# Kernel optimization log

Hardware: AMD Instinct MI355X
Metric: run time of the kernel (lower is better)

## Reference

```python
import jax, jax.numpy as jnp
import numpy as np

V, D, H, L, B, S = 32000, 512, 512, 2, 64, 64
PAD = 0
NEG = -1000000000.0


def setup_inputs() -> dict:
    key = jax.random.key(0)
    ks = jax.random.split(key, 12)
    s = 0.05
    X = jax.random.randint(ks[0], (B, S), 0, V)
    enc = jax.random.normal(ks[1], (B, S - 1, H), jnp.float32)
    mask = jnp.zeros((S - 1, S - 1), dtype=bool)
    emb = jax.random.normal(ks[2], (V, D), jnp.float32) * s
    lstm_Wih = jax.random.normal(ks[3], (L, 4 * H, D), jnp.float32) * s  # D == H so stacking works for layer>0
    lstm_Whh = jax.random.normal(ks[4], (L, 4 * H, H), jnp.float32) * s
    lstm_bih = jax.random.normal(ks[5], (L, 4 * H), jnp.float32) * s
    lstm_bhh = jax.random.normal(ks[6], (L, 4 * H), jnp.float32) * s
    attn_Wh = jax.random.normal(ks[7], (H, H), jnp.float32) * s  # attn weight cols acting on decoder hidden
    attn_We = jax.random.normal(ks[8], (H, H), jnp.float32) * s  # attn weight cols acting on encoder outputs
    attn_b = jax.random.normal(ks[9], (H,), jnp.float32) * s
    v_w = jax.random.normal(ks[10], (H,), jnp.float32) * s
    fc_W = jax.random.normal(ks[11], (V, 2 * H), jnp.float32) * s
    fc_b = jnp.zeros((V,), jnp.float32)
    return {"X": X, "encoderOutputs": enc, "mask": mask, "emb": emb,
            "lstm_Wih": lstm_Wih, "lstm_Whh": lstm_Whh, "lstm_bih": lstm_bih, "lstm_bhh": lstm_bhh,
            "attn_Wh": attn_Wh, "attn_We": attn_We, "attn_b": attn_b, "v_w": v_w,
            "fc_W": fc_W, "fc_b": fc_b}


def _forward(X, enc, mask, emb, Wih, Whh, bih, bhh, attn_Wh, attn_We, attn_b, v_w, fc_W, fc_b):
    Bn, Sn = X.shape
    T = Sn - 1
    E = emb[X[:, :-1]]  # [B,T,D]
    # encoder part of attention projection is time-invariant: hoist out of the loop
    enc_proj = jnp.einsum('beh,kh->bek', enc, attn_We) + attn_b  # [B,T,H]
    h0 = jnp.zeros((L, Bn, H), E.dtype)
    c0 = jnp.zeros((L, Bn, H), E.dtype)
    xs = (jnp.transpose(E, (1, 0, 2)), X[:, 1:].T, jnp.arange(T))

    def step(carry, x_t):
        h, c = carry
        e_t, tgt, t = x_t
        inp = e_t
        hs, cs = [], []
        for l in range(L):  # fixed small layer loop
            g = inp @ Wih[l].T + h[l] @ Whh[l].T + bih[l] + bhh[l]
            i, f, gg, o = jnp.split(g, 4, axis=-1)  # torch gate order i,f,g,o
            cn = jax.nn.sigmoid(f) * c[l] + jax.nn.sigmoid(i) * jnp.tanh(gg)
            hn = jax.nn.sigmoid(o) * jnp.tanh(cn)
            hs.append(hn); cs.append(cn)
            inp = hn
        h = jnp.stack(hs); c = jnp.stack(cs)
        top = inp  # [B,H] == LSTM output of last layer
        energy = jnp.tanh((top @ attn_Wh.T)[:, None, :] + enc_proj)  # [B,T,H]
        scores = energy @ v_w  # [B,T]
        # original: self.mask[t-1] (python negative wrap) then mask.unsqueeze(0).unsqueeze(1)
        m = mask[(t - 1) % mask.shape[0], :T]  # [T]
        s3 = jnp.where(m[None, None, :], NEG, scores[None])  # broadcast -> [1,B,T]
        att = jax.nn.softmax(s3, axis=1)[0]  # softmax over batch dim, as in original
        weighted = jnp.einsum('be,beh->bh', att, enc)
        logits = jnp.concatenate([top, weighted], axis=1) @ fc_W.T + fc_b  # [B,V]
        logp = jax.nn.log_softmax(logits, axis=-1)
        nll = -jnp.take_along_axis(logp, tgt[:, None], axis=1)[:, 0]
        valid = tgt != PAD
        loss_t = jnp.sum(jnp.where(valid, nll, 0.0)) / jnp.sum(valid)  # CE mean with ignore_index
        return (h, c), loss_t

    _, losses = jax.lax.scan(step, (h0, c0), xs)
    return jnp.mean(losses)  # totalLoss / (seq_len - 1)


def reference(X, encoderOutputs, mask, emb, lstm_Wih, lstm_Whh, lstm_bih, lstm_bhh, attn_Wh, attn_We, attn_b, v_w, fc_W, fc_b):
    return _forward(X, encoderOutputs, mask, emb, lstm_Wih, lstm_Whh, lstm_bih, lstm_bhh, attn_Wh, attn_We, attn_b, v_w, fc_W, fc_b)
```

## Files before the change

kernel.cpp:

```cpp
#include <hip/hip_runtime.h>
#include <math.h>

#define NEGV -1000000000.0f

typedef unsigned short u16;
typedef __attribute__((ext_vector_type(8))) short bf16x8;
typedef __attribute__((ext_vector_type(4))) float f32x4;

__device__ __forceinline__ u16 f2bf(float f){
  union { float f; unsigned u; } v; v.f = f;
  unsigned u = v.u;
  unsigned r = (u + 0x7fffu + ((u >> 16) & 1u)) >> 16;
  return (u16)r;
}
__device__ __forceinline__ float bf2f(u16 b){
  union { unsigned u; float f; } v; v.u = ((unsigned)b) << 16;
  return v.f;
}
__device__ __forceinline__ float sigmf(float x){ return 1.f / (1.f + __expf(-x)); }
__device__ __forceinline__ float tanhf_(float x){
  float e = __expf(-2.f * fabsf(x));
  float t = (1.f - e) / (1.f + e);
  return x >= 0.f ? t : -t;
}
__device__ __forceinline__ float wred64(float v){
  #pragma unroll
  for (int m = 32; m; m >>= 1) v += __shfl_xor(v, m, 64);
  return v;
}
__device__ __forceinline__ float wmax64(float v){
  #pragma unroll
  for (int m = 32; m; m >>= 1) v = fmaxf(v, __shfl_xor(v, m, 64));
  return v;
}

typedef const __attribute__((address_space(1))) unsigned int* gas_ptr;
typedef __attribute__((address_space(3))) unsigned int* las_ptr;
__device__ __forceinline__ void gl_lds16(const u16* g, u16* l){
  __builtin_amdgcn_global_load_lds((gas_ptr)g, (las_ptr)l, 16, 0, 0);
}

__device__ __forceinline__ void st_sc1_u16(u16* p, unsigned v){
  asm volatile("global_store_short %0, %1, off sc1" :: "v"(p), "v"(v) : "memory");
}

__global__ __launch_bounds__(256) void k_prep(
    const float* wih, const float* whh, const float* we, const float* wh,
    const float* fcw, const float* enc, const float* bih, const float* bhh,
    u16* wihb, u16* whhb, u16* web, u16* whb, u16* fcwb, u16* encb, float* b01)
{
  const long n0 = 2097152, n1 = 2097152, n2 = 262144, n3 = 262144;
  const long n4 = 32768000, n5 = 2064384, n6 = 4096;
  const long total = n0 + n1 + n2 + n3 + n4 + n5 + n6;
  long stride = (long)gridDim.x * 256;
  for (long i = (long)blockIdx.x * 256 + threadIdx.x; i < total; i += stride){
    long j = i;
    if (j < n0){ wihb[j] = f2bf(wih[j]); continue; } j -= n0;
    if (j < n1){ whhb[j] = f2bf(whh[j]); continue; } j -= n1;
    if (j < n2){ web[j]  = f2bf(we[j]);  continue; } j -= n2;
    if (j < n3){ whb[j]  = f2bf(wh[j]);  continue; } j -= n3;
    if (j < n4){ fcwb[j] = f2bf(fcw[j]); continue; } j -= n4;
    if (j < n5){ encb[j] = f2bf(enc[j]); continue; } j -= n5;
    b01[j] = bih[j] + bhh[j];
  }
}

__global__ __launch_bounds__(256) void k_embed(const int* X, const float* emb, u16* ebf){
  int row = blockIdx.x;
  int t = row >> 6, b = row & 63;
  int tok = X[b * 64 + t];
  const float* src = emb + (long)tok * 512;
  u16* dst = ebf + (long)row * 512;
  for (int j = threadIdx.x; j < 512; j += 256) dst[j] = f2bf(src[j]);
}

__global__ __launch_bounds__(256) void gemm_bt(
    const u16* Am, int lda, const u16* Bm, int ldb,
    float* C, int ldc, const float* bias, int K)
{
  __shared__ u16 sA[64 * 32], sB[64 * 32];
  int tm = blockIdx.x, tn = blockIdx.y;
  int tid = threadIdx.x;
  int wave = tid >> 6, lane = tid & 63;
  int wm = wave >> 1, wn = wave & 1;
  int q = lane >> 4, cl = lane & 15;
  f32x4 acc[2][2];
  #pragma unroll
  for (int i = 0; i < 2; i++)
    #pragma unroll
    for (int j = 0; j < 2; j++) acc[i][j] = (f32x4){0.f, 0.f, 0.f, 0.f};

  int r = tid >> 2, ck = tid & 3;
  const u16* Ags = Am + (long)(tm * 64 + r) * lda + ck * 8;
  const u16* Bgs = Bm + (long)(tn * 64 + r) * ldb + ck * 8;
  u16* sAw = &sA[wave * 512];
  u16* sBw = &sB[wave * 512];

  for (int kt = 0; kt < K; kt += 32){
    gl_lds16(Ags + kt, sAw);
    gl_lds16(Bgs + kt, sBw);
    __syncthreads();
    #pragma unroll
    for (int i = 0; i < 2; i++){
      bf16x8 af = *(const bf16x8*)&sA[(wm * 32 + i * 16 + cl) * 32 + q * 8];
      #pragma unroll
      for (int j = 0; j < 2; j++){
        bf16x8 bfv = *(const bf16x8*)&sB[(wn * 32 + j * 16 + cl) * 32 + q * 8];
        acc[i][j] = __builtin_amdgcn_mfma_f32_16x16x32_bf16(af, bfv, acc[i][j], 0, 0, 0);
      }
    }
    __syncthreads();
  }
  #pragma unroll
  for (int i = 0; i < 2; i++)
    #pragma unroll
    for (int j = 0; j < 2; j++){
      int colg = tn * 64 + wn * 32 + j * 16 + cl;
      float bv = bias ? bias[colg] : 0.f;
      #pragma unroll
      for (int rr = 0; rr < 4; rr++){
        int rowg = tm * 64 + wm * 32 + i * 16 + q * 4 + rr;
        C[(long)rowg * ldc + colg] = acc[i][j][rr] + bv;
      }
    }
}

__global__ __launch_bounds__(256) void gemm_btb(
    const u16* Am, int lda, const u16* Bm, int ldb,
    u16* C, int ldc, const float* bias, int K)
{
  __shared__ u16 sA[64 * 32], sB[64 * 32];
  int tm = blockIdx.x, tn = blockIdx.y;
  int tid = threadIdx.x;
  int wave = tid >> 6, lane = tid & 63;
  int wm = wave >> 1, wn = wave & 1;
  int q = lane >> 4, cl = lane & 15;
  f32x4 acc[2][2];
  #pragma unroll
  for (int i = 0; i < 2; i++)
    #pragma unroll
    for (int j = 0; j < 2; j++) acc[i][j] = (f32x4){0.f, 0.f, 0.f, 0.f};

  int r = tid >> 2, ck = tid & 3;
  const u16* Ags = Am + (long)(tm * 64 + r) * lda + ck * 8;
  const u16* Bgs = Bm + (long)(tn * 64 + r) * ldb + ck * 8;
  u16* sAw = &sA[wave * 512];
  u16* sBw = &sB[wave * 512];

  for (int kt = 0; kt < K; kt += 32){
    gl_lds16(Ags + kt, sAw);
    gl_lds16(Bgs + kt, sBw);
    __syncthreads();
    #pragma unroll
    for (int i = 0; i < 2; i++){
      bf16x8 af = *(const bf16x8*)&sA[(wm * 32 + i * 16 + cl) * 32 + q * 8];
      #pragma unroll
      for (int j = 0; j < 2; j++){
        bf16x8 bfv = *(const bf16x8*)&sB[(wn * 32 + j * 16 + cl) * 32 + q * 8];
        acc[i][j] = __builtin_amdgcn_mfma_f32_16x16x32_bf16(af, bfv, acc[i][j], 0, 0, 0);
      }
    }
    __syncthreads();
  }
  #pragma unroll
  for (int i = 0; i < 2; i++)
    #pragma unroll
    for (int j = 0; j < 2; j++){
      int colg = tn * 64 + wn * 32 + j * 16 + cl;
      float bv = bias ? bias[colg] : 0.f;
      #pragma unroll
      for (int rr = 0; rr < 4; rr++){
        int rowg = tm * 64 + wm * 32 + i * 16 + q * 4 + rr;
        C[(long)rowg * ldc + colg] = f2bf(acc[i][j][rr] + bv);
      }
    }
}

__device__ __forceinline__ void wait_flags(int* flags, int tid, int need0, int need1){
  if (tid < 64){
    int need = (tid < 32) ? need0 : need1;
    for (;;){
      int v = __hip_atomic_load(flags + tid, __ATOMIC_RELAXED, __HIP_MEMORY_SCOPE_AGENT);
      if (__ballot(v >= need) == ~0ull) break;
    }
  }
  __syncthreads();
}

#define LOAD_RING_FRAGS(afr, Ab)                                              \
  {                                                                            \
    _Pragma("unroll")                                                          \
    for (int kt = 0; kt < 16; kt++)                                            \
      asm volatile("global_load_dwordx4 %0, %1, off offset:%2 sc1"             \
                   : "=v"(afr[kt]) : "v"(Ab), "i"(kt * 64));                   \
    asm volatile("s_waitcnt vmcnt(0)" ::: "memory");                           \
    __builtin_amdgcn_sched_barrier(0);                                         \
  }

__global__ __launch_bounds__(256, 1) void lstm_pipe(
    const u16* whh0, const u16* wih1, const u16* whh1,
    const u16* x0b, const float* b1s,
    u16* ring0, u16* ring1, u16* feat, int* flags)
{
  __shared__ u16 sW[32768];
  __shared__ u16 sW2[32768];
  int wg = blockIdx.x;
  int layer = wg >> 5;
  int cc = (wg & 31) * 16;
  int tid = threadIdx.x;
  int wave = tid >> 6, lane = tid & 63;
  int q = lane >> 4, cl = lane & 15;
  int j = cc + cl;

  {
    const u16* src = layer ? whh1 : whh0;
    for (int ch = tid; ch < 4096; ch += 256){
      int row = ch >> 6, c = ch & 63;
      int g = row >> 4, r = row & 15;
      *(uint4*)&sW[((c * 4 + g) * 16 + r) * 8] =
          *(const uint4*)&src[(long)(g * 512 + cc + r) * 512 + c * 8];
      if (layer)
        *(uint4*)&sW2[((c * 4 + g) * 16 + r) * 8] =
            *(const uint4*)&wih1[(long)(g * 512 + cc + r) * 512 + c * 8];
    }
  }
  __syncthreads();

  float cst[4] = {0.f, 0.f, 0.f, 0.f};
  float bg[4];
  if (layer){
    #pragma unroll
    for (int g = 0; g < 4; g++) bg[g] = b1s[g * 512 + j];
  }

  const int LOW = -(1 << 30);

  for (int t = 0; t < 63; t++){
    f32x4 acc[4];
    #pragma unroll
    for (int g = 0; g < 4; g++) acc[g] = (f32x4){0.f, 0.f, 0.f, 0.f};

    if (layer == 0){
      float xg[4][4];
      #pragma unroll
      for (int rr = 0; rr < 4; rr++){
        int s = wave * 16 + q * 4 + rr;
        const u16* xr = x0b + (long)(t * 64 + s) * 2048 + j;
        #pragma unroll
        for (int g = 0; g < 4; g++) xg[g][rr] = bf2f(xr[g * 512]);
      }
      wait_flags(flags, tid, t, t - 3);
      {
        const u16* Ab = ring0 + ((t + 3) & 3) * 32768 + (wave * 16 + cl) * 512 + q * 8;
        bf16x8 afr[16];
        LOAD_RING_FRAGS(afr, Ab);
        #pragma unroll
        for (int kt = 0; kt < 16; kt++)
          #pragma unroll
          for (int g = 0; g < 4; g++){
            bf16x8 bfv = *(const bf16x8*)&sW[(((kt * 4 + q) * 4 + g) * 16 + cl) * 8];
            acc[g] = __builtin_amdgcn_mfma_f32_16x16x32_bf16(afr[kt], bfv, acc[g], 0, 0, 0);
          }
      }
      u16* hn = ring0 + (t & 3) * 32768;
      #pragma unroll
      for (int rr = 0; rr < 4; rr++){
        int s = wave * 16 + q * 4 + rr;
        float gi = acc[0][rr] + xg[0][rr];
        float gf = acc[1][rr] + xg[1][rr];
        float gg = acc[2][rr] + xg[2][rr];
        float go = acc[3][rr] + xg[3][rr];
        float cn = sigmf(gf) * cst[rr] + sigmf(gi) * tanhf_(gg);
        cst[rr] = cn;
        st_sc1_u16(hn + s * 512 + j, (unsigned)f2bf(sigmf(go) * tanhf_(cn)));
      }
    } else {
      wait_flags(flags, tid, LOW, t);
      {
        const u16* Ab = ring1 + ((t + 3) & 3) * 32768 + (wave * 16 + cl) * 512 + q * 8;
        bf16x8 afr[16];
        LOAD_RING_FRAGS(afr, Ab);
        #pragma unroll
        for (int kt = 0; kt < 16; kt++)
          #pragma unroll
          for (int g = 0; g < 4; g++){
            bf16x8 bfv = *(const bf16x8*)&sW[(((kt * 4 + q) * 4 + g) * 16 + cl) * 8];
            acc[g] = __builtin_amdgcn_mfma_f32_16x16x32_bf16(afr[kt], bfv, acc[g], 0, 0, 0);
          }
      }
      wait_flags(flags, tid, t + 1, LOW);
      {
        const u16* Ab = ring0 + (t & 3) * 32768 + (wave * 16 + cl) * 512 + q * 8;
        bf16x8 afr[16];
        LOAD_RING_FRAGS(afr, Ab);
        #pragma unroll
        for (int kt = 0; kt < 16; kt++)
          #pragma unroll
          for (int g = 0; g < 4; g++){
            bf16x8 bfv = *(const bf16x8*)&sW2[(((kt * 4 + q) * 4 + g) * 16 + cl) * 8];
            acc[g] = __builtin_amdgcn_mfma_f32_16x16x32_bf16(afr[kt], bfv, acc[g], 0, 0, 0);
          }
      }
      u16* hn = ring1 + (t & 3) * 32768;
      #pragma unroll
      for (int rr = 0; rr < 4; rr++){
        int s = wave * 16 + q * 4 + rr;
        float gi = acc[0][rr] + bg[0];
        float gf = acc[1][rr] + bg[1];
        float gg = acc[2][rr] + bg[2];
        float go = acc[3][rr] + bg[3];
        float cn = sigmf(gf) * cst[rr] + sigmf(gi) * tanhf_(gg);
        cst[rr] = cn;
        u16 hb = f2bf(sigmf(go) * tanhf_(cn));
        st_sc1_u16(hn + s * 512 + j, (unsigned)hb);
        feat[(long)(t * 64 + s) * 1024 + j] = hb;
      }
    }
    asm volatile("s_waitcnt vmcnt(0)" ::: "memory");
    __syncthreads();
    if (tid == 0)
      __hip_atomic_store(flags + wg, t + 1, __ATOMIC_RELAXED, __HIP_MEMORY_SCOPE_AGENT);
  }
}

__global__ __launch_bounds__(256) void k_scores(
    const float* qb, const float* encp, const float* vw, float* scores)
{
  int row = blockIdx.x;
  int b = row & 63;
  int wave = threadIdx.x >> 6, lane = threadIdx.x & 63;
  float qv[8], vwv[8];
  const float* qr = qb + (long)row * 512 + lane * 8;
  #pragma unroll
  for (int i = 0; i < 8; i++){ qv[i] = qr[i]; vwv[i] = vw[lane * 8 + i]; }
  for (int e = wave; e < 63; e += 4){
    const float* er = encp + (long)(b * 63 + e) * 512 + lane * 8;
    float s = 0.f;
    #pragma unroll
    for (int i = 0; i < 8; i++) s += vwv[i] * tanhf_(qv[i] + er[i]);
    s = wred64(s);
    if (lane == 0) scores[(long)row * 63 + e] = s;
  }
}

__global__ __launch_bounds__(64) void k_att(float* scores, const unsigned char* mask){
  int idx = blockIdx.x;
  int t = idx / 63, e = idx - t * 63;
  int lane = threadIdx.x;
  long off = (long)(t * 64 + lane) * 63 + e;
  float s = scores[off];
  if (mask[((t + 62) % 63) * 63 + e]) s = NEGV;
  float M = wmax64(s);
  float p = __expf(s - M);
  float S = wred64(p);
  scores[off] = p / S;
}

__global__ __launch_bounds__(256) void k_weighted(
    const float* att, const float* enc, u16* feat)
{
  int row = blockIdx.x;
  int b = row & 63;
  int j = threadIdx.x;
  float a0 = 0.f, a1 = 0.f;
  const float* ar = att + (long)row * 63;
  const float* er = enc + (long)b * 63 * 512;
  for (int e = 0; e < 63; e++){
    float a = ar[e];
    a0 += a * er[(long)e * 512 + j];
    a1 += a * er[(long)e * 512 + j + 256];
  }
  feat[(long)row * 1024 + 512 + j] = f2bf(a0);
  feat[(long)row * 1024 + 768 + j] = f2bf(a1);
}

__global__ __launch_bounds__(256) void gemm_fc(
    const u16* Am, const u16* Bm, const float* fcb, float* partials)
{
  __shared__ u16 sA[128 * 32], sB[128 * 32];
  __shared__ float sm[128][2], ss[128][2];
  int tm = blockIdx.x, tn = blockIdx.y;
  int tid = threadIdx.x;
  int wave = tid >> 6, lane = tid & 63;
  int wm = wave >> 1, wn = wave & 1;
  int q = lane >> 4, cl = lane & 15;
  f32x4 acc[4][4];
  #pragma unroll
  for (int i = 0; i < 4; i++)
    #pragma unroll
    for (int j = 0; j < 4; j++) acc[i][j] = (f32x4){0.f, 0.f, 0.f, 0.f};

  const u16 *Ag[2], *Bg[2];
  u16 *sAd[2], *sBd[2];
  #pragma unroll
  for (int h = 0; h < 2; h++){
    int idx = h * 256 + tid, rr = idx >> 2, ck = idx & 3;
    Ag[h] = Am + (long)(tm * 128 + rr) * 1024 + ck * 8;
    Bg[h] = Bm + (long)(tn * 128 + rr) * 1024 + ck * 8;
    sAd[h] = &sA[(h * 4 + wave) * 512];
    sBd[h] = &sB[(h * 4 + wave) * 512];
  }
  for (int kt = 0; kt < 1024; kt += 32){
    #pragma unroll
    for (int h = 0; h < 2; h++){
      gl_lds16(Ag[h] + kt, sAd[h]);
      gl_lds16(Bg[h] + kt, sBd[h]);
    }
    __syncthreads();
    bf16x8 afr[4];
    #pragma unroll
    for (int mt = 0; mt < 4; mt++)
      afr[mt] = *(const bf16x8*)&sA[(wm * 64 + mt * 16 + cl) * 32 + q * 8];
    #pragma unroll
    for (int nt = 0; nt < 4; nt++){
      bf16x8 bfv = *(const bf16x8*)&sB[(wn * 64 + nt * 16 + cl) * 32 + q * 8];
      #pragma unroll
      for (int mt = 0; mt < 4; mt++)
        acc[mt][nt] = __builtin_amdgcn_mfma_f32_16x16x32_bf16(afr[mt], bfv, acc[mt][nt], 0, 0, 0);
    }
    __syncthreads();
  }
  float fb[4];
  #pragma unroll
  for (int nt = 0; nt < 4; nt++) fb[nt] = fcb[tn * 128 + wn * 64 + nt * 16 + cl];
  #pragma unroll
  for (int mt = 0; mt < 4; mt++){
    #pragma unroll
    for (int rr = 0; rr < 4; rr++){
      float vals[4];
      float vm = -3.0e38f, vs = 0.f;
      #pragma unroll
      for (int nt = 0; nt < 4; nt++){ float v = acc[mt][nt][rr] + fb[nt]; vals[nt] = v; vm = fmaxf(vm, v); }
      #pragma unroll
      for (int nt = 0; nt < 4; nt++) vs += __expf(vals[nt] - vm);
      #pragma unroll
      for (int m = 1; m < 16; m <<= 1){
        float om = __shfl_xor(vm, m, 16);
        float os = __shfl_xor(vs, m, 16);
        float nm = fmaxf(vm, om);
        vs = vs * __expf(vm - nm) + os * __expf(om - nm);
        vm = nm;
      }
      if (cl == 0){ int rl = wm * 64 + mt * 16 + q * 4 + rr; sm[rl][wn] = vm; ss[rl][wn] = vs; }
    }
  }
  __syncthreads();
  if (tid < 128){
    float m0 = sm[tid][0], m1 = sm[tid][1];
    float M = fmaxf(m0, m1);
    float S = ss[tid][0] * __expf(m0 - M) + ss[tid][1] * __expf(m1 - M);
    long row = tm * 128 + tid;
    partials[(row * 250 + tn) * 2]     = M;
    partials[(row * 250 + tn) * 2 + 1] = S;
  }
}

__global__ __launch_bounds__(256) void k_rowstats(
    const float* partials, const u16* feat, const u16* fcwb,
    const float* fcb, const int* X, float* nll)
{
  int row = blockIdx.x * 4 + (threadIdx.x >> 6);
  int lane = threadIdx.x & 63;
  if (row >= 4032) return;
  float vm = -3.0e38f, vs = 0.f;
  const float* pr = partials + (long)row * 500;
  for (int i = lane; i < 250; i += 64){
    float m = pr[i * 2], s2 = pr[i * 2 + 1];
    float nm = fmaxf(vm, m);
    vs = vs * __expf(vm - nm) + s2 * __expf(m - nm);
    vm = nm;
  }
  #pragma unroll
  for (int m = 32; m; m >>= 1){
    float om = __shfl_xor(vm, m, 64);
    float os = __shfl_xor(vs, m, 64);
    float nm = fmaxf(vm, om);
    vs = vs * __expf(vm - nm) + os * __expf(om - nm);
    vm = nm;
  }
  float logZ = vm + __logf(vs);
  int t = row >> 6, b = row & 63;
  int tgt = X[b * 64 + t + 1];
  const u16* fr = feat + (long)row * 1024 + lane * 16;
  const u16* wr = fcwb + (long)tgt * 1024 + lane * 16;
  float d = 0.f;
  #pragma unroll
  for (int i = 0; i < 16; i++) d += bf2f(fr[i]) * bf2f(wr[i]);
  d = wred64(d);
  if (lane == 0) nll[row] = logZ - (d + fcb[tgt]);
}

__global__ __launch_bounds__(256) void k_final(const float* nll, const int* X, float* out){
  __shared__ float lt[64];
  int wave = threadIdx.x >> 6, lane = threadIdx.x & 63;
  for (int t = wave; t < 63; t += 4){
    int tgt = X[lane * 64 + t + 1];
    float v = (tgt != 0) ? nll[t * 64 + lane] : 0.f;
    float c = (tgt != 0) ? 1.f : 0.f;
    v = wred64(v); c = wred64(c);
    if (lane == 0) lt[t] = v / c;
  }
  __syncthreads();
  if (threadIdx.x == 0){
    float s = 0.f;
    for (int t = 0; t < 63; t++) s += lt[t];
    out[0] = s / 63.f;
  }
}

extern "C" void kernel_launch(void* const* d_in, const int* in_sizes, int n_in,
                              void* d_out, int out_size, void* d_ws, size_t ws_size,
                              hipStream_t stream)
{
  (void)in_sizes; (void)n_in; (void)out_size; (void)ws_size;
  const int*   X    = (const int*)d_in[0];
  const float* enc  = (const float*)d_in[1];
  const unsigned char* mask = (const unsigned char*)d_in[2];
  const float* emb  = (const float*)d_in[3];
  const float* wih  = (const float*)d_in[4];
  const float* whh  = (const float*)d_in[5];
  const float* bih  = (const float*)d_in[6];
  const float* bhh  = (const float*)d_in[7];
  const float* awh  = (const float*)d_in[8];
  const float* awe  = (const float*)d_in[9];
  const float* ab   = (const float*)d_in[10];
  const float* vw   = (const float*)d_in[11];
  const float* fcw  = (const float*)d_in[12];
  const float* fcb  = (const float*)d_in[13];
  float* out = (float*)d_out;

  char* w = (char*)d_ws;
  size_t o = 0;
  auto alloc = [&](size_t bytes){ size_t r = o; o = (o + bytes + 255) & ~(size_t)255; return r; };
  size_t o_ebf  = alloc((size_t)4032 * 512 * 2);
  size_t o_wihb = alloc((size_t)2 * 2048 * 512 * 2);
  size_t o_whhb = alloc((size_t)2 * 2048 * 512 * 2);
  size_t o_web  = alloc((size_t)512 * 512 * 2);
  size_t o_whb  = alloc((size_t)512 * 512 * 2);
  size_t o_fcwb = alloc((size_t)32000 * 1024 * 2);
  size_t o_encb = alloc((size_t)4032 * 512 * 2);
  size_t o_b01  = alloc((size_t)4096 * 4);
  size_t o_x0   = alloc((size_t)4032 * 2048 * 2);
  size_t o_encp = alloc((size_t)4032 * 512 * 4);
  size_t o_q    = alloc((size_t)4032 * 512 * 4);
  size_t o_feat = alloc((size_t)4096 * 1024 * 2);
  size_t o_ring = alloc((size_t)2 * 4 * 32768 * 2);
  size_t o_flags= alloc((size_t)256);
  size_t o_sc   = alloc((size_t)63 * 64 * 63 * 4);
  size_t o_part = alloc((size_t)4096 * 250 * 2 * 4);
  size_t o_nll  = alloc((size_t)4032 * 4);

  u16* ebf   = (u16*)(w + o_ebf);
  u16* wihb  = (u16*)(w + o_wihb);
  u16* whhb  = (u16*)(w + o_whhb);
  u16* web   = (u16*)(w + o_web);
  u16* whb   = (u16*)(w + o_whb);
  u16* fcwb  = (u16*)(w + o_fcwb);
  u16* encb  = (u16*)(w + o_encb);
  float* b01 = (float*)(w + o_b01);
  u16* x0b   = (u16*)(w + o_x0);
  float* encp= (float*)(w + o_encp);
  float* qb  = (float*)(w + o_q);
  u16* feat  = (u16*)(w + o_feat);
  u16* ring0 = (u16*)(w + o_ring);
  u16* ring1 = ring0 + 4 * 32768;
  int* flags = (int*)(w + o_flags);
  float* sc  = (float*)(w + o_sc);
  float* part= (float*)(w + o_part);
  float* nllb= (float*)(w + o_nll);

  hipMemsetAsync(w + o_ring, 0, (o_flags - o_ring) + 256, stream);

  k_prep<<<4096, 256, 0, stream>>>(wih, whh, awe, awh, fcw, enc, bih, bhh,
                                   wihb, whhb, web, whb, fcwb, encb, b01);
  k_embed<<<4032, 256, 0, stream>>>(X, emb, ebf);

  gemm_btb<<<dim3(63, 32), 256, 0, stream>>>(ebf, 512, wihb, 512, x0b, 2048, b01, 512);
  gemm_bt<<<dim3(63, 8), 256, 0, stream>>>(encb, 512, web, 512, encp, 512, ab, 512);

  lstm_pipe<<<64, 256, 0, stream>>>(whhb, wihb + 2048 * 512, whhb + 2048 * 512,
                                    x0b, b01 + 2048, ring0, ring1, feat, flags);

  gemm_bt<<<dim3(63, 8), 256, 0, stream>>>(feat, 1024, whb, 512, qb, 512, nullptr, 512);
  k_scores<<<4032, 256, 0, stream>>>(qb, encp, vw, sc);
  k_att<<<3969, 64, 0, stream>>>(sc, mask);
  k_weighted<<<4032, 256, 0, stream>>>(sc, enc, feat);

  gemm_fc<<<dim3(32, 250), 256, 0, stream>>>(feat, fcwb, fcb, part);
  k_rowstats<<<1008, 256, 0, stream>>>(part, feat, fcwb, fcb, X, nllb);
  k_final<<<1, 256, 0, stream>>>(nllb, X, out);
}
```

Measured before the change: 1.363 ms.

## Deepen LSTM ring buffer to 8 and merge layer-1 flag waits with overlapped loads

The ring buffers carrying hidden states between the two LSTM layers' workgroups grow from 4 to 8 slots, so layer 0 can run up to 7 steps ahead of layer 1 instead of 3. Layer 1 now waits once for both its own previous step and layer 0's current step, then issues both sets of fragment loads together. It partially waits on the vmcnt counter so the first MFMA chain overlaps the second load. This removes a serial flag-wait and load latency from the recurrent critical path. The cost is a combined wait that may stall layer 1 longer when layer 0 lags, plus a larger ring footprint.

Result: faster. 1.298 ms (-4.7%).

```diff
diff --git a/kernel.cpp b/kernel.cpp
--- a/kernel.cpp
+++ b/kernel.cpp
@@ -187,15 +187,16 @@
   __syncthreads();
 }
 
-#define LOAD_RING_FRAGS(afr, Ab)                                              \
+#define ISSUE_RING_FRAGS(afr, Ab)                                              \
   {                                                                            \
     _Pragma("unroll")                                                          \
     for (int kt = 0; kt < 16; kt++)                                            \
       asm volatile("global_load_dwordx4 %0, %1, off offset:%2 sc1"             \
                    : "=v"(afr[kt]) : "v"(Ab), "i"(kt * 64));                   \
-    asm volatile("s_waitcnt vmcnt(0)" ::: "memory");                           \
-    __builtin_amdgcn_sched_barrier(0);                                         \
-  }
+  }
+#define WAITCNT_VM(N)                                                          \
+  { asm volatile("s_waitcnt vmcnt(" #N ")" ::: "memory");                      \
+    __builtin_amdgcn_sched_barrier(0); }
 
 __global__ __launch_bounds__(256, 1) void lstm_pipe(
     const u16* whh0, const u16* wih1, const u16* whh1,
@@ -233,7 +234,7 @@
     for (int g = 0; g < 4; g++) bg[g] = b1s[g * 512 + j];
   }
 
-  const int LOW = -(1 << 30);
+  int foff = (wave * 16 + cl) * 512 + q * 8;
 
   for (int t = 0; t < 63; t++){
     f32x4 acc[4];
@@ -249,11 +250,12 @@
         #pragma unroll
         for (int g = 0; g < 4; g++) xg[g][rr] = bf2f(xr[g * 512]);
       }
-      wait_flags(flags, tid, t, t - 3);
+      wait_flags(flags, tid, t, t - 7);
       {
-        const u16* Ab = ring0 + ((t + 3) & 3) * 32768 + (wave * 16 + cl) * 512 + q * 8;
+        const u16* Ab = ring0 + ((t + 7) & 7) * 32768 + foff;
         bf16x8 afr[16];
-        LOAD_RING_FRAGS(afr, Ab);
+        ISSUE_RING_FRAGS(afr, Ab);
+        WAITCNT_VM(0);
         #pragma unroll
         for (int kt = 0; kt < 16; kt++)
           #pragma unroll
@@ -262,7 +264,7 @@
             acc[g] = __builtin_amdgcn_mfma_f32_16x16x32_bf16(afr[kt], bfv, acc[g], 0, 0, 0);
           }
       }
-      u16* hn = ring0 + (t & 3) * 32768;
+      u16* hn = ring0 + (t & 7) * 32768;
       #pragma unroll
       for (int rr = 0; rr < 4; rr++){
         int s = wave * 16 + q * 4 + rr;
@@ -275,33 +277,29 @@
         st_sc1_u16(hn + s * 512 + j, (unsigned)f2bf(sigmf(go) * tanhf_(cn)));
       }
     } else {
-      wait_flags(flags, tid, LOW, t);
-      {
-        const u16* Ab = ring1 + ((t + 3) & 3) * 32768 + (wave * 16 + cl) * 512 + q * 8;
-        bf16x8 afr[16];
-        LOAD_RING_FRAGS(afr, Ab);
+      wait_flags(flags, tid, t + 1, t);
+      const u16* Ab1 = ring1 + ((t + 7) & 7) * 32768 + foff;
+      const u16* Ab0 = ring0 + (t & 7) * 32768 + foff;
+      bf16x8 a1[16], a0[16];
+      ISSUE_RING_FRAGS(a1, Ab1);
+      ISSUE_RING_FRAGS(a0, Ab0);
+      WAITCNT_VM(16);
+      #pragma unroll
+      for (int kt = 0; kt < 16; kt++)
         #pragma unroll
-        for (int kt = 0; kt < 16; kt++)
-          #pragma unroll
-          for (int g = 0; g < 4; g++){
-            bf16x8 bfv = *(const bf16x8*)&sW[(((kt * 4 + q) * 4 + g) * 16 + cl) * 8];
-            acc[g] = __builtin_amdgcn_mfma_f32_16x16x32_bf16(afr[kt], bfv, acc[g], 0, 0, 0);
-          }
-      }
-      wait_flags(flags, tid, t + 1, LOW);
-      {
-        const u16* Ab = ring0 + (t & 3) * 32768 + (wave * 16 + cl) * 512 + q * 8;
-        bf16x8 afr[16];
-        LOAD_RING_FRAGS(afr, Ab);
+        for (int g = 0; g < 4; g++){
+          bf16x8 bfv = *(const bf16x8*)&sW[(((kt * 4 + q) * 4 + g) * 16 + cl) * 8];
+          acc[g] = __builtin_amdgcn_mfma_f32_16x16x32_bf16(a1[kt], bfv, acc[g], 0, 0, 0);
+        }
+      WAITCNT_VM(0);
+      #pragma unroll
+      for (int kt = 0; kt < 16; kt++)
         #pragma unroll
-        for (int kt = 0; kt < 16; kt++)
-          #pragma unroll
-          for (int g = 0; g < 4; g++){
-            bf16x8 bfv = *(const bf16x8*)&sW2[(((kt * 4 + q) * 4 + g) * 16 + cl) * 8];
-            acc[g] = __builtin_amdgcn_mfma_f32_16x16x32_bf16(afr[kt], bfv, acc[g], 0, 0, 0);
-          }
-      }
-      u16* hn = ring1 + (t & 3) * 32768;
+        for (int g = 0; g < 4; g++){
+          bf16x8 bfv = *(const bf16x8*)&sW2[(((kt * 4 + q) * 4 + g) * 16 + cl) * 8];
+          acc[g] = __builtin_amdgcn_mfma_f32_16x16x32_bf16(a0[kt], bfv, acc[g], 0, 0, 0);
+        }
+      u16* hn = ring1 + (t & 7) * 32768;
       #pragma unroll
       for (int rr = 0; rr < 4; rr++){
         int s = wave * 16 + q * 4 + rr;
@@ -544,7 +542,7 @@
   size_t o_encp = alloc((size_t)4032 * 512 * 4);
   size_t o_q    = alloc((size_t)4032 * 512 * 4);
   size_t o_feat = alloc((size_t)4096 * 1024 * 2);
-  size_t o_ring = alloc((size_t)2 * 4 * 32768 * 2);
+  size_t o_ring = alloc((size_t)2 * 8 * 32768 * 2);
   size_t o_flags= alloc((size_t)256);
   size_t o_sc   = alloc((size_t)63 * 64 * 63 * 4);
   size_t o_part = alloc((size_t)4096 * 250 * 2 * 4);
@@ -563,7 +561,7 @@
   float* qb  = (float*)(w + o_q);
   u16* feat  = (u16*)(w + o_feat);
   u16* ring0 = (u16*)(w + o_ring);
-  u16* ring1 = ring0 + 4 * 32768;
+  u16* ring1 = ring0 + 8 * 32768;
   int* flags = (int*)(w + o_flags);
   float* sc  = (float*)(w + o_sc);
   float* part= (float*)(w + o_part);
```
